# Performance work log

Hardware: AMD Instinct MI355X
Metric: run time of the kernel (lower is better)

The kernel has to match this reference:

```python
import jax, jax.numpy as jnp
import numpy as np
import math

C_IN = 256
INTER = 64  # max(256//4, 8)
MAX_SIZE = 64
TEMP = 1.0


def setup_inputs() -> dict:
    key = jax.random.key(0)
    ks = jax.random.split(key, 12)
    B, C, H, W = 16, C_IN, 64, 64
    x = jax.random.normal(ks[0], (B, C, H, W), dtype=jnp.float32)
    pos_embedding = jax.random.normal(ks[1], (1, INTER, MAX_SIZE, MAX_SIZE), dtype=jnp.float32) * 0.02
    # 1x1 conv weights stored as [out, in] (kernel spatial dims are 1)
    def xavier(k, out_c, in_c):
        bound = math.sqrt(6.0 / (in_c + out_c))
        return jax.random.uniform(k, (out_c, in_c), dtype=jnp.float32, minval=-bound, maxval=bound)
    wq = xavier(ks[2], INTER, C)
    wk = xavier(ks[3], INTER, C)
    wv = xavier(ks[4], INTER, C)
    wo = xavier(ks[5], C, INTER)
    bq = jnp.zeros((INTER,), jnp.float32)
    bk = jnp.zeros((INTER,), jnp.float32)
    bv = jnp.zeros((INTER,), jnp.float32)
    bo = jnp.zeros((C,), jnp.float32)
    gamma = jnp.ones((1,), jnp.float32) * 0.1
    return {"x": x, "pos_embedding": pos_embedding, "wq": wq, "bq": bq,
            "wk": wk, "bk": bk, "wv": wv, "bv": bv, "wo": wo, "bo": bo,
            "gamma": gamma}


def reference(x, pos_embedding, wq, bq, wk, bk, wv, bv, wo, bo, gamma):
    B, C, H, W = x.shape
    N = H * W
    pos = pos_embedding[:, :, :H, :W]  # [1, INTER, H, W]

    def conv1x1(w, b, inp):
        # [out,in] x [B,in,H,W] -> [B,out,H,W]
        return jnp.einsum('oc,bchw->bohw', w, inp) + b[None, :, None, None]

    q = conv1x1(wq, bq, x) + pos
    k = conv1x1(wk, bk, x) + pos
    v = conv1x1(wv, bv, x)

    # flatten spatial -> tokens: [B, N, INTER]
    q = q.reshape(B, INTER, N).transpose(0, 2, 1)
    k = k.reshape(B, INTER, N).transpose(0, 2, 1)
    v = v.reshape(B, INTER, N).transpose(0, 2, 1)

    scale = 1.0 / (TEMP * math.sqrt(INTER))
    logits = jnp.einsum('bnd,bmd->bnm', q, k) * scale  # [B, N, N]
    attn = jax.nn.softmax(logits, axis=-1)
    attended = jnp.einsum('bnm,bmd->bnd', attn, v)  # [B, N, INTER]

    attended = attended.transpose(0, 2, 1).reshape(B, INTER, H, W)
    out = conv1x1(wo, bo, attended)
    return gamma * out + x
```

## Files before the change

### kernel.cpp

```cpp
#include <hip/hip_runtime.h>

typedef unsigned short u16;
typedef unsigned int u32;
typedef __attribute__((ext_vector_type(8))) short short8;
typedef __attribute__((ext_vector_type(4))) float f32x4;
typedef __attribute__((ext_vector_type(16))) float f32x16;

#define DEV static __device__ __forceinline__

DEV u16 f2bf(float f) {
  u32 u = __builtin_bit_cast(u32, f);
  u += 0x7FFFu + ((u >> 16) & 1u);
  return (u16)(u >> 16);
}
DEV u32 cvtpk(float a, float b) {
  u32 d;
  asm("v_cvt_pk_bf16_f32 %0, %1, %2" : "=v"(d) : "v"(a), "v"(b));
  return d;
}
DEV short8 ld8(const u16* p) {
  uint4 v = *reinterpret_cast<const uint4*>(p);
  return __builtin_bit_cast(short8, v);
}

DEV short8 frag8(const float* p) {
  u32 a0 = cvtpk(p[0], p[1]);
  u32 a1 = cvtpk(p[2], p[3]);
  u32 b0 = cvtpk(p[4], p[5]);
  u32 b1 = cvtpk(p[6], p[7]);
  asm("v_permlane32_swap_b32 %0, %1" : "+v"(a0), "+v"(b0));
  asm("v_permlane32_swap_b32 %0, %1" : "+v"(a1), "+v"(b1));
  uint4 u;
  u.x = a0; u.y = a1; u.z = b0; u.w = b1;
  return __builtin_bit_cast(short8, u);
}

#define BB 16
#define CC 256
#define DD 64
#define NN 4096

__global__ __launch_bounds__(256) void prep_kernel(
    const float* __restrict__ wq, const float* __restrict__ wk,
    const float* __restrict__ wv, const float* __restrict__ wo,
    u16* __restrict__ wqb, u16* __restrict__ wkb,
    u16* __restrict__ wvb, u16* __restrict__ wob)
{
  int i = blockIdx.x * 256 + threadIdx.x;
  wqb[i] = f2bf(wq[i]);
  wkb[i] = f2bf(wk[i]);
  wvb[i] = f2bf(wv[i]);
  wob[i] = f2bf(wo[i]);
}

__global__ __launch_bounds__(256, 4) void qkv_kernel(
    const float* __restrict__ xg, const float* __restrict__ pos_e,
    const u16* __restrict__ wqb, const u16* __restrict__ wkb,
    const u16* __restrict__ wvb,
    const float* __restrict__ bq, const float* __restrict__ bk,
    const float* __restrict__ bv,
    u16* __restrict__ Qb, u16* __restrict__ Kb, u16* __restrict__ Vt)
{
  const int nc = blockIdx.x, b = blockIdx.y, tid = threadIdx.x;
  const int n0 = nc * 64;
  __shared__ u16 Xs[64 * 256];

  {
    const int ng = tid & 15;
    const int ch0 = tid >> 4;
#pragma unroll
    for (int it = 0; it < 2; ++it) {
      const int c0 = (ch0 + 16 * it) * 8;
      f32x4 xv[8];
#pragma unroll
      for (int j = 0; j < 8; ++j)
        xv[j] = *reinterpret_cast<const f32x4*>(
            xg + ((size_t)(b * CC + c0 + j)) * NN + n0 + ng * 4);
#pragma unroll
      for (int i = 0; i < 4; ++i) {
        const int n = ng * 4 + i;
        uint4 o;
        o.x = cvtpk(xv[0][i], xv[1][i]);
        o.y = cvtpk(xv[2][i], xv[3][i]);
        o.z = cvtpk(xv[4][i], xv[5][i]);
        o.w = cvtpk(xv[6][i], xv[7][i]);
        *reinterpret_cast<uint4*>(&Xs[n * 256 + (c0 ^ ((n & 7) * 8))]) = o;
      }
    }
  }
  __syncthreads();

  const int w = tid >> 6, lane = tid & 63, lc = lane & 15, quad = lane >> 4;
  const int swz = (lc & 7) * 8;

  const u16* wsp[3];
  int gsel[3];
#pragma unroll
  for (int j = 0; j < 3; ++j) {
    const int nt = w * 3 + j;
    wsp[j] = (nt < 4) ? wqb : (nt < 8) ? wkb : wvb;
    gsel[j] = nt & 3;
  }

  f32x4 acc[3][4];
#pragma unroll
  for (int j = 0; j < 3; ++j)
#pragma unroll
    for (int ns = 0; ns < 4; ++ns) acc[j][ns] = (f32x4){0.f, 0.f, 0.f, 0.f};

#pragma unroll
  for (int kk = 0; kk < 8; ++kk) {
    short8 bf[3], af[4];
#pragma unroll
    for (int j = 0; j < 3; ++j)
      bf[j] = ld8(wsp[j] + (size_t)(gsel[j] * 16 + lc) * CC + kk * 32 + quad * 8);
#pragma unroll
    for (int ns = 0; ns < 4; ++ns)
      af[ns] = ld8(&Xs[(ns * 16 + lc) * 256 + ((kk * 32 + quad * 8) ^ swz)]);
#pragma unroll
    for (int j = 0; j < 3; ++j) {
      const int nt = w * 3 + j;
#pragma unroll
      for (int ns = 0; ns < 4; ++ns) {
        if (nt < 8)
          acc[j][ns] = __builtin_amdgcn_mfma_f32_16x16x32_bf16(bf[j], af[ns], acc[j][ns], 0, 0, 0);
        else
          acc[j][ns] = __builtin_amdgcn_mfma_f32_16x16x32_bf16(af[ns], bf[j], acc[j][ns], 0, 0, 0);
      }
    }
  }

  __syncthreads();
  u16* Vst = Xs;

#pragma unroll
  for (int j = 0; j < 3; ++j) {
    const int nt = w * 3 + j;
    if (nt < 8) {
      u16* dst = (nt < 4) ? Qb : Kb;
      const float* bsrc = (nt < 4) ? bq : bk;
      const int ch0 = gsel[j] * 16 + quad * 4;
      const f32x4 bias4 = *reinterpret_cast<const f32x4*>(bsrc + ch0);
#pragma unroll
      for (int ns = 0; ns < 4; ++ns) {
        const int n = n0 + ns * 16 + lc;
        float v[4];
#pragma unroll
        for (int r = 0; r < 4; ++r) {
          v[r] = acc[j][ns][r] + bias4[r] + pos_e[(size_t)(ch0 + r) * NN + n];
          if (nt < 4) v[r] *= 0.125f;
        }
        uint2 o2;
        o2.x = cvtpk(v[0], v[1]);
        o2.y = cvtpk(v[2], v[3]);
        *reinterpret_cast<uint2*>(&dst[((size_t)(b * NN + n)) * DD + ch0]) = o2;
      }
    } else {
      const int ch = gsel[j] * 16 + lc;
      const float bias = bv[ch];
#pragma unroll
      for (int ns = 0; ns < 4; ++ns) {
        uint2 o2;
        o2.x = cvtpk(acc[j][ns][0] + bias, acc[j][ns][1] + bias);
        o2.y = cvtpk(acc[j][ns][2] + bias, acc[j][ns][3] + bias);
        *reinterpret_cast<uint2*>(
            &Vst[ch * 64 + ((ns * 16 + quad * 4) ^ ((ch & 7) * 8))]) = o2;
      }
    }
  }
  __syncthreads();

  {
    const int ch = tid >> 2, part = tid & 3;
    const int sw = (ch & 7) * 8;
    const uint4 a  = *reinterpret_cast<const uint4*>(&Vst[ch * 64 + ((part * 16) ^ sw)]);
    const uint4 c2 = *reinterpret_cast<const uint4*>(&Vst[ch * 64 + ((part * 16 + 8) ^ sw)]);
    u16* dst = Vt + ((size_t)(b * DD + ch)) * NN + n0 + part * 16;
    *reinterpret_cast<uint4*>(dst) = a;
    *reinterpret_cast<uint4*>(dst + 8) = c2;
  }
}

#define QB 128

__global__ __launch_bounds__(512, 4) void flash_kernel(
    const u16* __restrict__ Qg, const u16* __restrict__ Kg,
    const u16* __restrict__ Vtg,
    const u16* __restrict__ wob, const float* __restrict__ bo,
    const float* __restrict__ gam, const float* __restrict__ xg,
    float* __restrict__ outg)
{
  const int qt = blockIdx.x, b = blockIdx.y, tid = threadIdx.x;
  const int w = tid >> 6, lane = tid & 63;
  const int l31 = lane & 31, hi8 = (lane >> 5) * 8;
  const int swz = (l31 & 7) * 8;
  const int khalf = w >> 2;
  const int qg = w & 3;

  __shared__ u16 pool[25088];
  u16* const KsA = pool;
  u16* const VsA = pool + 8192;
  u16* const AttS = pool + 16384;
  float* const poolF = reinterpret_cast<float*>(pool);

  const u16* Kbase = Kg + (size_t)b * NN * DD;
  const u16* Vbase = Vtg + (size_t)b * DD * NN;

  const int sr = tid >> 3, seg = (tid & 7) * 8;
  const int sdst = sr * 64 + (seg ^ ((sr & 7) * 8));
  const u16* kp = Kbase + (size_t)sr * DD + seg;
  const u16* vp = Vbase + (size_t)sr * NN + seg;

  const int qrow = qt * QB + qg * 32 + l31;
  short8 qf[4];
#pragma unroll
  for (int kk = 0; kk < 4; ++kk)
    qf[kk] = ld8(Qg + ((size_t)(b * NN + qrow)) * DD + kk * 16 + hi8);

  uint4 kr = *reinterpret_cast<const uint4*>(kp);
  uint4 vr = *reinterpret_cast<const uint4*>(vp);
  *reinterpret_cast<uint4*>(&KsA[sdst]) = kr;
  *reinterpret_cast<uint4*>(&VsA[sdst]) = vr;
  __syncthreads();

  f32x16 O0 = (f32x16)0.0f;
  f32x16 O1 = (f32x16)0.0f;
  float lsum = 0.f;

  for (int kt = 0; kt < 64; ++kt) {
    const int cur = kt & 1;
    if (kt < 63) {
      kr = *reinterpret_cast<const uint4*>(kp + (size_t)(kt + 1) * (64 * DD));
      vr = *reinterpret_cast<const uint4*>(vp + (kt + 1) * 64);
    }
    const u16* Kc = KsA + cur * 4096;
    const u16* Vc = VsA + cur * 4096;

    f32x16 S = (f32x16)0.0f;
    __builtin_amdgcn_s_setprio(1);
#pragma unroll
    for (int kk = 0; kk < 4; ++kk) {
      short8 af = ld8(&Kc[(khalf * 32 + l31) * 64 + ((kk * 16 + hi8) ^ swz)]);
      S = __builtin_amdgcn_mfma_f32_32x32x16_bf16(af, qf[kk], S, 0, 0, 0);
    }
    __builtin_amdgcn_s_setprio(0);

    float p[16];
#pragma unroll
    for (int r = 0; r < 16; ++r) {
      float e = __expf(fminf(S[r], 80.f));
      p[r] = e;
      lsum += e;
    }

    short8 pf0 = frag8(&p[0]);
    short8 pf1 = frag8(&p[8]);

    __builtin_amdgcn_s_setprio(1);
#pragma unroll
    for (int kf = 0; kf < 2; ++kf) {
      const short8 pfv = kf ? pf1 : pf0;
      const int ko = (khalf * 32 + kf * 16 + hi8) ^ swz;
      short8 v0 = ld8(&Vc[l31 * 64 + ko]);
      O0 = __builtin_amdgcn_mfma_f32_32x32x16_bf16(v0, pfv, O0, 0, 0, 0);
      short8 v1 = ld8(&Vc[(32 + l31) * 64 + ko]);
      O1 = __builtin_amdgcn_mfma_f32_32x32x16_bf16(v1, pfv, O1, 0, 0, 0);
    }
    __builtin_amdgcn_s_setprio(0);

    if (kt < 63) {
      const int nxt = cur ^ 1;
      *reinterpret_cast<uint4*>(&KsA[nxt * 4096 + sdst]) = kr;
      *reinterpret_cast<uint4*>(&VsA[nxt * 4096 + sdst]) = vr;
      __syncthreads();
    }
  }

  __syncthreads();

  lsum += __shfl_xor(lsum, 32);

  if (w >= 4) {
    const int base = ((w - 4) * 64 + lane) * 32;
#pragma unroll
    for (int i = 0; i < 4; ++i) {
      f32x4 t0 = {O0[i * 4 + 0], O0[i * 4 + 1], O0[i * 4 + 2], O0[i * 4 + 3]};
      *reinterpret_cast<f32x4*>(&poolF[base + ((i * 4) ^ ((lane & 7) * 4))]) = t0;
      f32x4 t1 = {O1[i * 4 + 0], O1[i * 4 + 1], O1[i * 4 + 2], O1[i * 4 + 3]};
      *reinterpret_cast<f32x4*>(&poolF[base + ((16 + i * 4) ^ ((lane & 7) * 4))]) = t1;
    }
    poolF[12288 + (w - 4) * 64 + lane] = lsum;
  }
  __syncthreads();

  if (w < 4) {
    const int base = (w * 64 + lane) * 32;
#pragma unroll
    for (int i = 0; i < 4; ++i) {
      f32x4 t0 = *reinterpret_cast<const f32x4*>(&poolF[base + ((i * 4) ^ ((lane & 7) * 4))]);
      f32x4 t1 = *reinterpret_cast<const f32x4*>(&poolF[base + ((16 + i * 4) ^ ((lane & 7) * 4))]);
#pragma unroll
      for (int j = 0; j < 4; ++j) {
        O0[i * 4 + j] += t0[j];
        O1[i * 4 + j] += t1[j];
      }
    }
    lsum += poolF[12288 + w * 64 + lane];
    const float rl = 1.0f / lsum;

    const int nl = w * 32 + l31;
    float a[16];
#pragma unroll
    for (int r = 0; r < 16; ++r) a[r] = O0[r] * rl;
    short8 f0 = frag8(&a[0]);
    short8 f1 = frag8(&a[8]);
    *reinterpret_cast<uint4*>(&AttS[nl * 64 + ((0 + hi8) ^ swz)]) =
        __builtin_bit_cast(uint4, f0);
    *reinterpret_cast<uint4*>(&AttS[nl * 64 + ((16 + hi8) ^ swz)]) =
        __builtin_bit_cast(uint4, f1);
#pragma unroll
    for (int r = 0; r < 16; ++r) a[r] = O1[r] * rl;
    f0 = frag8(&a[0]);
    f1 = frag8(&a[8]);
    *reinterpret_cast<uint4*>(&AttS[nl * 64 + ((32 + hi8) ^ swz)]) =
        __builtin_bit_cast(uint4, f0);
    *reinterpret_cast<uint4*>(&AttS[nl * 64 + ((48 + hi8) ^ swz)]) =
        __builtin_bit_cast(uint4, f1);
  }
  __syncthreads();

  const int lc = lane & 15, quad = lane >> 4;
  const int swz16 = (lc & 7) * 8;
  f32x4 acc[2][8];
#pragma unroll
  for (int i = 0; i < 2; ++i)
#pragma unroll
    for (int j = 0; j < 8; ++j) acc[i][j] = (f32x4){0.f, 0.f, 0.f, 0.f};

#pragma unroll
  for (int kk = 0; kk < 2; ++kk) {
    short8 bfr[8];
#pragma unroll
    for (int nt = 0; nt < 8; ++nt)
      bfr[nt] = ld8(&AttS[(nt * 16 + lc) * 64 + ((kk * 32 + quad * 8) ^ swz16)]);
#pragma unroll
    for (int mti = 0; mti < 2; ++mti) {
      short8 af = ld8(wob + (size_t)(w * 32 + mti * 16 + lc) * DD + kk * 32 + quad * 8);
#pragma unroll
      for (int nt = 0; nt < 8; ++nt)
        acc[mti][nt] = __builtin_amdgcn_mfma_f32_16x16x32_bf16(af, bfr[nt], acc[mti][nt], 0, 0, 0);
    }
  }

  const float g = gam[0];
  const int n0 = qt * QB;
#pragma unroll
  for (int mti = 0; mti < 2; ++mti)
#pragma unroll
    for (int rr = 0; rr < 4; ++rr) {
      const int co = w * 32 + mti * 16 + quad * 4 + rr;
      const float bov = bo[co];
#pragma unroll
      for (int nt = 0; nt < 8; ++nt) {
        const int n = n0 + nt * 16 + lc;
        const size_t idx = ((size_t)(b * CC + co)) * NN + n;
        outg[idx] = g * (acc[mti][nt][rr] + bov) + xg[idx];
      }
    }
}

extern "C" void kernel_launch(void* const* d_in, const int* in_sizes, int n_in,
                              void* d_out, int out_size, void* d_ws, size_t ws_size,
                              hipStream_t stream) {
  const float* x   = (const float*)d_in[0];
  const float* pos = (const float*)d_in[1];
  const float* wq  = (const float*)d_in[2];
  const float* bq  = (const float*)d_in[3];
  const float* wk  = (const float*)d_in[4];
  const float* bk  = (const float*)d_in[5];
  const float* wv  = (const float*)d_in[6];
  const float* bv  = (const float*)d_in[7];
  const float* wo  = (const float*)d_in[8];
  const float* bo  = (const float*)d_in[9];
  const float* gm  = (const float*)d_in[10];
  float* out = (float*)d_out;

  u16* Qb  = (u16*)d_ws;
  u16* Kb  = Qb + (size_t)BB * NN * DD;
  u16* Vt  = Kb + (size_t)BB * NN * DD;
  u16* wqb = Vt + (size_t)BB * NN * DD;
  u16* wkb = wqb + 16384;
  u16* wvb = wkb + 16384;
  u16* wob = wvb + 16384;

  dim3 blk(256);
  prep_kernel<<<dim3(64), blk, 0, stream>>>(wq, wk, wv, wo, wqb, wkb, wvb, wob);
  qkv_kernel<<<dim3(64, 16), blk, 0, stream>>>(x, pos, wqb, wkb, wvb, bq, bk, bv, Qb, Kb, Vt);
  flash_kernel<<<dim3(32, 16), dim3(512), 0, stream>>>(Qb, Kb, Vt, wob, bo, gm, x, out);
}
```

Before: 247.6 us.

## Double KV tile to 128 keys per step and fold log2e into Q scale

The flash attention kernel now stages 128 keys per iteration instead of 64. That halves the number of loop iterations and block-wide barriers, and each wave computes two 32x32 score tiles per step, using a new 16-slot XOR swizzle for the wider V rows. The Q pre-scale now includes log2(e), so the softmax can use exp2f instead of __expf. LDS per block grows from about 49KB to 64KB, which may lower the number of resident blocks at 512 threads each.

After: 273.3 us. +10.4%, slower.

```diff
diff --git a/kernel.cpp b/kernel.cpp
--- a/kernel.cpp
+++ b/kernel.cpp
@@ -39,6 +39,8 @@
 #define CC 256
 #define DD 64
 #define NN 4096
+
+#define QSCALE 0.18033688011112042f
 
 __global__ __launch_bounds__(256) void prep_kernel(
     const float* __restrict__ wq, const float* __restrict__ wk,
@@ -148,7 +150,7 @@
 #pragma unroll
         for (int r = 0; r < 4; ++r) {
           v[r] = acc[j][ns][r] + bias4[r] + pos_e[(size_t)(ch0 + r) * NN + n];
-          if (nt < 4) v[r] *= 0.125f;
+          if (nt < 4) v[r] *= QSCALE;
         }
         uint2 o2;
         o2.x = cvtpk(v[0], v[1]);
@@ -182,6 +184,7 @@
 }
 
 #define QB 128
+#define KVB 128
 
 __global__ __launch_bounds__(512, 4) void flash_kernel(
     const u16* __restrict__ Qg, const u16* __restrict__ Kg,
@@ -193,21 +196,23 @@
   const int qt = blockIdx.x, b = blockIdx.y, tid = threadIdx.x;
   const int w = tid >> 6, lane = tid & 63;
   const int l31 = lane & 31, hi8 = (lane >> 5) * 8;
-  const int swz = (l31 & 7) * 8;
   const int khalf = w >> 2;
   const int qg = w & 3;
 
-  __shared__ u16 pool[25088];
+  __shared__ u16 pool[32768];
   u16* const KsA = pool;
-  u16* const VsA = pool + 8192;
+  u16* const VsA = pool + 16384;
   u16* const AttS = pool + 16384;
   float* const poolF = reinterpret_cast<float*>(pool);
 
   const u16* Kbase = Kg + (size_t)b * NN * DD;
   const u16* Vbase = Vtg + (size_t)b * DD * NN;
 
-  const int sr = tid >> 3, seg = (tid & 7) * 8;
-  const int sdst = sr * 64 + (seg ^ ((sr & 7) * 8));
+  const int sr = tid >> 3, s0 = tid & 7, seg = s0 * 8;
+  const int kd0 = sr * 64 + (seg ^ ((sr & 7) * 8));
+  const int kd1 = (sr + 64) * 64 + (seg ^ ((sr & 7) * 8));
+  const int vd0 = sr * 128 + ((s0 ^ (sr & 15)) * 8);
+  const int vd1 = sr * 128 + (((s0 + 8) ^ (sr & 15)) * 8);
   const u16* kp = Kbase + (size_t)sr * DD + seg;
   const u16* vp = Vbase + (size_t)sr * NN + seg;
 
@@ -217,61 +222,76 @@
   for (int kk = 0; kk < 4; ++kk)
     qf[kk] = ld8(Qg + ((size_t)(b * NN + qrow)) * DD + kk * 16 + hi8);
 
-  uint4 kr = *reinterpret_cast<const uint4*>(kp);
-  uint4 vr = *reinterpret_cast<const uint4*>(vp);
-  *reinterpret_cast<uint4*>(&KsA[sdst]) = kr;
-  *reinterpret_cast<uint4*>(&VsA[sdst]) = vr;
+  uint4 kra = *reinterpret_cast<const uint4*>(kp);
+  uint4 krb = *reinterpret_cast<const uint4*>(kp + 64 * DD);
+  uint4 vra = *reinterpret_cast<const uint4*>(vp);
+  uint4 vrb = *reinterpret_cast<const uint4*>(vp + 64);
+  *reinterpret_cast<uint4*>(&KsA[kd0]) = kra;
+  *reinterpret_cast<uint4*>(&KsA[kd1]) = krb;
+  *reinterpret_cast<uint4*>(&VsA[vd0]) = vra;
+  *reinterpret_cast<uint4*>(&VsA[vd1]) = vrb;
   __syncthreads();
 
   f32x16 O0 = (f32x16)0.0f;
   f32x16 O1 = (f32x16)0.0f;
   float lsum = 0.f;
 
-  for (int kt = 0; kt < 64; ++kt) {
+  for (int kt = 0; kt < NN / KVB; ++kt) {
     const int cur = kt & 1;
-    if (kt < 63) {
-      kr = *reinterpret_cast<const uint4*>(kp + (size_t)(kt + 1) * (64 * DD));
-      vr = *reinterpret_cast<const uint4*>(vp + (kt + 1) * 64);
-    }
-    const u16* Kc = KsA + cur * 4096;
-    const u16* Vc = VsA + cur * 4096;
-
-    f32x16 S = (f32x16)0.0f;
+    if (kt < NN / KVB - 1) {
+      const size_t ko = (size_t)(kt + 1) * KVB;
+      kra = *reinterpret_cast<const uint4*>(kp + ko * DD);
+      krb = *reinterpret_cast<const uint4*>(kp + ko * DD + 64 * DD);
+      vra = *reinterpret_cast<const uint4*>(vp + ko);
+      vrb = *reinterpret_cast<const uint4*>(vp + ko + 64);
+    }
+    const u16* Kc = KsA + cur * 8192;
+    const u16* Vc = VsA + cur * 8192;
+
+    f32x16 S0 = (f32x16)0.0f, S1 = (f32x16)0.0f;
     __builtin_amdgcn_s_setprio(1);
 #pragma unroll
     for (int kk = 0; kk < 4; ++kk) {
-      short8 af = ld8(&Kc[(khalf * 32 + l31) * 64 + ((kk * 16 + hi8) ^ swz)]);
-      S = __builtin_amdgcn_mfma_f32_32x32x16_bf16(af, qf[kk], S, 0, 0, 0);
+      const int co = (kk * 16 + hi8) ^ ((l31 & 7) * 8);
+      short8 a0 = ld8(&Kc[(khalf * 64 + l31) * 64 + co]);
+      S0 = __builtin_amdgcn_mfma_f32_32x32x16_bf16(a0, qf[kk], S0, 0, 0, 0);
+      short8 a1 = ld8(&Kc[(khalf * 64 + 32 + l31) * 64 + co]);
+      S1 = __builtin_amdgcn_mfma_f32_32x32x16_bf16(a1, qf[kk], S1, 0, 0, 0);
     }
     __builtin_amdgcn_s_setprio(0);
 
-    float p[16];
-#pragma unroll
-    for (int r = 0; r < 16; ++r) {
-      float e = __expf(fminf(S[r], 80.f));
-      p[r] = e;
-      lsum += e;
-    }
-
-    short8 pf0 = frag8(&p[0]);
-    short8 pf1 = frag8(&p[8]);
-
-    __builtin_amdgcn_s_setprio(1);
-#pragma unroll
-    for (int kf = 0; kf < 2; ++kf) {
-      const short8 pfv = kf ? pf1 : pf0;
-      const int ko = (khalf * 32 + kf * 16 + hi8) ^ swz;
-      short8 v0 = ld8(&Vc[l31 * 64 + ko]);
-      O0 = __builtin_amdgcn_mfma_f32_32x32x16_bf16(v0, pfv, O0, 0, 0, 0);
-      short8 v1 = ld8(&Vc[(32 + l31) * 64 + ko]);
-      O1 = __builtin_amdgcn_mfma_f32_32x32x16_bf16(v1, pfv, O1, 0, 0, 0);
-    }
-    __builtin_amdgcn_s_setprio(0);
-
-    if (kt < 63) {
+#pragma unroll
+    for (int kf2 = 0; kf2 < 2; ++kf2) {
+      const f32x16& Sx = kf2 ? S1 : S0;
+      float p[16];
+#pragma unroll
+      for (int r = 0; r < 16; ++r) {
+        float e = exp2f(fminf(Sx[r], 80.f));
+        p[r] = e;
+        lsum += e;
+      }
+      short8 pf0 = frag8(&p[0]);
+      short8 pf1 = frag8(&p[8]);
+
+      __builtin_amdgcn_s_setprio(1);
+#pragma unroll
+      for (int kf = 0; kf < 2; ++kf) {
+        const short8 pfv = kf ? pf1 : pf0;
+        const int slot = khalf * 8 + kf2 * 4 + kf * 2 + (hi8 >> 3);
+        short8 v0 = ld8(&Vc[l31 * 128 + ((slot ^ (l31 & 15)) * 8)]);
+        O0 = __builtin_amdgcn_mfma_f32_32x32x16_bf16(v0, pfv, O0, 0, 0, 0);
+        short8 v1 = ld8(&Vc[(32 + l31) * 128 + ((slot ^ (l31 & 15)) * 8)]);
+        O1 = __builtin_amdgcn_mfma_f32_32x32x16_bf16(v1, pfv, O1, 0, 0, 0);
+      }
+      __builtin_amdgcn_s_setprio(0);
+    }
+
+    if (kt < NN / KVB - 1) {
       const int nxt = cur ^ 1;
-      *reinterpret_cast<uint4*>(&KsA[nxt * 4096 + sdst]) = kr;
-      *reinterpret_cast<uint4*>(&VsA[nxt * 4096 + sdst]) = vr;
+      *reinterpret_cast<uint4*>(&KsA[nxt * 8192 + kd0]) = kra;
+      *reinterpret_cast<uint4*>(&KsA[nxt * 8192 + kd1]) = krb;
+      *reinterpret_cast<uint4*>(&VsA[nxt * 8192 + vd0]) = vra;
+      *reinterpret_cast<uint4*>(&VsA[nxt * 8192 + vd1]) = vrb;
       __syncthreads();
     }
   }
@@ -309,6 +329,7 @@
     const float rl = 1.0f / lsum;
 
     const int nl = w * 32 + l31;
+    const int swz = (l31 & 7) * 8;
     float a[16];
 #pragma unroll
     for (int r = 0; r < 16; ++r) a[r] = O0[r] * rl;
```
